# Optimization experiments

Measured on AMD Instinct MI355X. Metric: run time of the kernel, lower is better.

## Reference

```python
import jax, jax.numpy as jnp
import numpy as np


def fwht(x):
    """Normalized fast Walsh-Hadamard transform over the last dim (power of 2).
    Equivalent to x @ H_n / sqrt(n) with H symmetric, so it serves as both
    matmul_hadU and matmul_hadUt in QuIP#."""
    n = x.shape[-1]
    steps = int(np.log2(n))
    assert 1 << steps == n
    shape = x.shape
    x = x.reshape(-1, n)
    h = 1
    for _ in range(steps):
        x = x.reshape(-1, n // (2 * h), 2, h)
        a = x[:, :, 0, :]
        b = x[:, :, 1, :]
        x = jnp.stack([a + b, a - b], axis=2).reshape(-1, n)
        h *= 2
    return (x * np.float32(1.0 / np.sqrt(n))).reshape(shape)


def setup_inputs() -> dict:
    key = jax.random.key(0)
    ks = jax.random.split(key, 9)
    B, S = 4, 2048
    n_in, n_out, codesz, cb_size, rank = 4096, 4096, 4, 256, 64
    inputs = {
        "input": jax.random.normal(ks[0], (B, S, n_in), dtype=jnp.float32),
        "Qidxs": jax.random.randint(ks[1], (n_out, n_in // codesz), 0, cb_size, dtype=jnp.int32),
        "D4_CB": jax.random.normal(ks[2], (cb_size, codesz), dtype=jnp.float32),
        # SU / SV are random sign (+-1) vectors from the randomized Hadamard transform
        "SU": jnp.where(jax.random.bernoulli(ks[3], 0.5, (n_in,)), 1.0, -1.0).astype(jnp.float32),
        "SV": jnp.where(jax.random.bernoulli(ks[4], 0.5, (n_out,)), 1.0, -1.0).astype(jnp.float32),
        "Wscale": jnp.float32(0.9),
        "A": jax.random.normal(ks[5], (n_out, rank), dtype=jnp.float32) * 0.02,
        "B": jax.random.normal(ks[6], (rank, n_in), dtype=jnp.float32) * 0.02,
        # positive per-input-channel rescale
        "scaleWH": jax.random.uniform(ks[7], (n_in,), dtype=jnp.float32, minval=0.5, maxval=1.5),
    }
    return inputs


def reference(input, Qidxs, D4_CB, SU, SV, Wscale, A, B, scaleWH):
    n_out, n_groups = Qidxs.shape
    codesz = D4_CB.shape[1]
    n_in = n_groups * codesz
    lead = input.shape[:-1]

    x = input.reshape(-1, n_in)            # [T, n_in]
    x = x / scaleWH                        # rescale_WH
    x = x * SU                             # input sign flips
    x = fwht(x)                            # matmul_hadUt
    Bx = x @ B.T                           # [T, rank] low-rank path

    # Dequantize: gather codebook vectors and flatten groups -> [n_out, n_in]
    W_hat = D4_CB[Qidxs].reshape(n_out, n_in)
    z = x @ W_hat.T                        # [T, n_out]

    z = z * Wscale
    z = z + Bx @ A.T                       # low-rank correction
    z = fwht(z)                            # matmul_hadU on output dim
    z = z * SV                             # output sign flips
    return z.reshape(*lead, n_out)
```

## Files before the change

kernel.cpp:

```cpp
#include <hip/hip_runtime.h>
#include <hip/hip_bf16.h>
#include <stdint.h>

typedef __attribute__((ext_vector_type(8))) short short8;
typedef __attribute__((ext_vector_type(4))) float floatx4;

#define GLOAD_LDS16(gptr, lptr)                                                     \
  __builtin_amdgcn_global_load_lds(                                                 \
      (const __attribute__((address_space(1))) void*)(gptr),                        \
      (__attribute__((address_space(3))) void*)(lptr), 16, 0, 0)

#define FENCE() asm volatile("" ::: "memory")
#define BARRIER() do { FENCE(); __builtin_amdgcn_s_barrier(); FENCE(); } while (0)
#define PHASE_END() do { __builtin_amdgcn_sched_barrier(0);                        \
                         asm volatile("s_waitcnt lgkmcnt(0)" ::: "memory");        \
                         __builtin_amdgcn_s_barrier();                             \
                         __builtin_amdgcn_sched_barrier(0); } while (0)

__device__ inline void fwht16(float v[16]) {
#pragma unroll
    for (int s = 0; s < 4; ++s) {
        const int h = 1 << s;
#pragma unroll
        for (int k = 0; k < 16; k += 2 * h)
#pragma unroll
            for (int j = 0; j < h; ++j) {
                float a = v[k + j], b = v[k + j + h];
                v[k + j] = a + b;
                v[k + j + h] = a - b;
            }
    }
}

__global__ __launch_bounds__(256) void decode_weff(
    const int* __restrict__ Qidxs, const float* __restrict__ D4_CB,
    const float* __restrict__ Wscale_p, const float* __restrict__ A,
    const float* __restrict__ B, __hip_bfloat16* __restrict__ W_eff)
{
    __shared__ __align__(16) float As[64 * 64];
    __shared__ __align__(16) float CB[256 * 4];
    const int t = threadIdx.x;
    const int oBase = blockIdx.y * 64;
    const int iBase = blockIdx.x * 256;

    const float4* A4 = (const float4*)(A + (long)oBase * 64);
    float4* As4 = (float4*)As;
#pragma unroll
    for (int u = 0; u < 4; ++u) As4[t + u * 256] = A4[t + u * 256];
    ((float4*)CB)[t] = ((const float4*)D4_CB)[t];
    __syncthreads();

    const float wscale = Wscale_p[0];
    const int i = iBase + t;
    float bcol[64];
#pragma unroll
    for (int r = 0; r < 64; ++r) bcol[r] = B[r * 4096 + i];

    const int g = i >> 2;
    const int sub = i & 3;

    for (int oo = 0; oo < 64; ++oo) {
        const int o = oBase + oo;
        const float4* arow = (const float4*)&As[oo * 64];
        float acc = 0.f;
#pragma unroll
        for (int r4 = 0; r4 < 16; ++r4) {
            float4 a4 = arow[r4];
            acc += a4.x * bcol[4 * r4 + 0] + a4.y * bcol[4 * r4 + 1] +
                   a4.z * bcol[4 * r4 + 2] + a4.w * bcol[4 * r4 + 3];
        }
        const int q = Qidxs[(long)o * 1024 + g];
        const float w = wscale * CB[q * 4 + sub] + acc;
        W_eff[(long)o * 4096 + i] = __float2bfloat16(w);
    }
}

__global__ __launch_bounds__(256) void fwht_in_kernel(
    const float* __restrict__ x, const float* __restrict__ SU,
    const float* __restrict__ sWH, __hip_bfloat16* __restrict__ xh)
{
    __shared__ float row[4096 + 256];
    const int t = threadIdx.x;
    const long base = (long)blockIdx.x * 4096;
    float v[16];

#pragma unroll
    for (int u = 0; u < 16; ++u) {
        int e = u * 256 + t;
        v[u] = x[base + e] / sWH[e] * SU[e];
    }
    fwht16(v);
#pragma unroll
    for (int u = 0; u < 16; ++u) {
        int e = u * 256 + t;
        row[e + (e >> 4)] = v[u];
    }
    __syncthreads();

    const int lo = t & 15, hi = t >> 4;
#pragma unroll
    for (int u = 0; u < 16; ++u) v[u] = row[hi * 272 + u * 17 + lo];
    fwht16(v);
#pragma unroll
    for (int u = 0; u < 16; ++u) row[hi * 272 + u * 17 + lo] = v[u];
    __syncthreads();

#pragma unroll
    for (int u = 0; u < 16; ++u) v[u] = row[t * 17 + u];
    fwht16(v);

    short8 o0, o1;
#pragma unroll
    for (int u = 0; u < 8; ++u) {
        __hip_bfloat16 b = __float2bfloat16(v[u] * 0.015625f);
        o0[u] = *(short*)&b;
    }
#pragma unroll
    for (int u = 0; u < 8; ++u) {
        __hip_bfloat16 b = __float2bfloat16(v[8 + u] * 0.015625f);
        o1[u] = *(short*)&b;
    }
    *(short8*)(xh + base + t * 16) = o0;
    *(short8*)(xh + base + t * 16 + 8) = o1;
}

__global__ __launch_bounds__(512, 2) void gemm_bt(
    const __hip_bfloat16* __restrict__ xh,
    const __hip_bfloat16* __restrict__ wf,
    __hip_bfloat16* __restrict__ z)
{
    __shared__ __align__(16) __hip_bfloat16 sA[2][256 * 64];
    __shared__ __align__(16) __hip_bfloat16 sB[2][256 * 64];

    const int t = threadIdx.x;
    const int lane = t & 63;
    const int wv = t >> 6;
    const int wm = wv >> 2;
    const int wn = wv & 3;
    const long mBase = (long)blockIdx.y * 256;
    const long nBase = (long)blockIdx.x * 256;

    const int grow = t >> 3;
    const int gcol = ((t & 7) ^ (grow & 7)) * 8;
    const __hip_bfloat16* gA = xh + (mBase + grow) * 4096 + gcol;
    const __hip_bfloat16* gB = wf + (nBase + grow) * 4096 + gcol;
    const int lrow = wv * 8;

    const int fr = lane & 15;
    const int c2 = lane >> 4;
    const int slot0 = ((c2 ^ (fr & 7)) * 8);

    floatx4 acc[8][4] = {};
    short8 afr[4][2];
    short8 bfr[4][2];

    auto stage = [&](int buf, int isA, int halfRow, int kt) {
        const __hip_bfloat16* g =
            (isA ? gA : gB) + (long)halfRow * 4096 + (long)kt * 64;
        __hip_bfloat16* l =
            (isA ? &sA[buf][0] : &sB[buf][0]) + (halfRow + lrow) * 64;
        GLOAD_LDS16(g, l);
        GLOAD_LDS16(g + 64L * 4096, l + 64 * 64);
    };
    auto ldA = [&](int buf, int mhalf) {
        const __hip_bfloat16* base =
            &sA[buf][0] + (wm * 128 + mhalf * 64 + fr) * 64;
#pragma unroll
        for (int m = 0; m < 4; ++m) {
            afr[m][0] = *(const short8*)(base + m * 16 * 64 + slot0);
            afr[m][1] = *(const short8*)(base + m * 16 * 64 + (slot0 ^ 32));
        }
    };
    auto ldB2 = [&](int buf, int npair) {
        const __hip_bfloat16* base =
            &sB[buf][0] + (wn * 64 + npair * 32 + fr) * 64;
#pragma unroll
        for (int n = 0; n < 2; ++n) {
            bfr[npair * 2 + n][0] = *(const short8*)(base + n * 16 * 64 + slot0);
            bfr[npair * 2 + n][1] = *(const short8*)(base + n * 16 * 64 + (slot0 ^ 32));
        }
    };
    auto mma16 = [&](int mh, int np) {
#pragma unroll
        for (int m = 0; m < 4; ++m)
#pragma unroll
            for (int n = 0; n < 2; ++n)
#pragma unroll
                for (int kh = 0; kh < 2; ++kh)
                    acc[mh * 4 + m][np * 2 + n] =
                        __builtin_amdgcn_mfma_f32_16x16x32_bf16(
                            afr[m][kh], bfr[np * 2 + n][kh],
                            acc[mh * 4 + m][np * 2 + n], 0, 0, 0);
    };

    stage(0, 1, 0,   0);
    stage(0, 1, 128, 0);
    stage(0, 0, 0,   0);
    stage(0, 0, 128, 0);
    stage(1, 0, 0,   1);
    stage(1, 1, 0,   1);
    asm volatile("s_waitcnt vmcnt(4)" ::: "memory");
    BARRIER();

    for (int kt = 0; kt < 64; ++kt) {
        const int cur = kt & 1;

        ldA(cur, 0);
        ldB2(cur, 0);
        if (kt + 1 < 64) stage(cur ^ 1, 1, 128, kt + 1);
        __builtin_amdgcn_s_setprio(1);
        mma16(0, 0);
        __builtin_amdgcn_s_setprio(0);
        PHASE_END();

        ldB2(cur, 1);
        if (kt + 1 < 64) stage(cur ^ 1, 0, 128, kt + 1);
        __builtin_amdgcn_s_setprio(1);
        mma16(0, 1);
        __builtin_amdgcn_s_setprio(0);
        PHASE_END();

        ldA(cur, 1);
        if (kt + 2 < 64) stage(cur, 0, 0, kt + 2);
        __builtin_amdgcn_s_setprio(1);
        mma16(1, 0);
        __builtin_amdgcn_s_setprio(0);
        PHASE_END();

        if (kt + 2 < 64) stage(cur, 1, 0, kt + 2);
        __builtin_amdgcn_s_setprio(1);
        mma16(1, 1);
        __builtin_amdgcn_s_setprio(0);
        __builtin_amdgcn_sched_barrier(0);
        if (kt < 62) asm volatile("s_waitcnt vmcnt(4) lgkmcnt(0)" ::: "memory");
        else         asm volatile("s_waitcnt vmcnt(0) lgkmcnt(0)" ::: "memory");
        __builtin_amdgcn_s_barrier();
        __builtin_amdgcn_sched_barrier(0);
    }

    const int q4 = c2 * 4;
#pragma unroll
    for (int m = 0; m < 8; ++m)
#pragma unroll
        for (int n = 0; n < 4; ++n)
#pragma unroll
            for (int r = 0; r < 4; ++r) {
                const long row = mBase + wm * 128 + m * 16 + q4 + r;
                const long col = nBase + wn * 64 + n * 16 + fr;
                z[row * 4096 + col] = __float2bfloat16(acc[m][n][r]);
            }
}

__global__ __launch_bounds__(256) void fwht_out_kernel(
    const __hip_bfloat16* __restrict__ z, const float* __restrict__ SV,
    float* __restrict__ out)
{
    __shared__ float row[4096 + 256];
    const int t = threadIdx.x;
    const long base = (long)blockIdx.x * 4096;
    float v[16];

#pragma unroll
    for (int u = 0; u < 16; ++u) {
        int e = u * 256 + t;
        v[u] = __bfloat162float(z[base + e]);
    }
    fwht16(v);
#pragma unroll
    for (int u = 0; u < 16; ++u) {
        int e = u * 256 + t;
        row[e + (e >> 4)] = v[u];
    }
    __syncthreads();

    const int lo = t & 15, hi = t >> 4;
#pragma unroll
    for (int u = 0; u < 16; ++u) v[u] = row[hi * 272 + u * 17 + lo];
    fwht16(v);
#pragma unroll
    for (int u = 0; u < 16; ++u) row[hi * 272 + u * 17 + lo] = v[u];
    __syncthreads();

#pragma unroll
    for (int u = 0; u < 16; ++u) v[u] = row[t * 17 + u];
    fwht16(v);

    const float4* svv = (const float4*)(SV + t * 16);
    float4* ov = (float4*)(out + base + t * 16);
#pragma unroll
    for (int c = 0; c < 4; ++c) {
        float4 s = svv[c];
        float4 f;
        f.x = v[4 * c + 0] * s.x * 0.015625f;
        f.y = v[4 * c + 1] * s.y * 0.015625f;
        f.z = v[4 * c + 2] * s.z * 0.015625f;
        f.w = v[4 * c + 3] * s.w * 0.015625f;
        ov[c] = f;
    }
}

extern "C" void kernel_launch(void* const* d_in, const int* in_sizes, int n_in,
                              void* d_out, int out_size, void* d_ws, size_t ws_size,
                              hipStream_t stream)
{
    const float* input  = (const float*)d_in[0];
    const int*   Qidxs  = (const int*)d_in[1];
    const float* D4_CB  = (const float*)d_in[2];
    const float* SU     = (const float*)d_in[3];
    const float* SV     = (const float*)d_in[4];
    const float* Wscale = (const float*)d_in[5];
    const float* A      = (const float*)d_in[6];
    const float* B      = (const float*)d_in[7];
    const float* sWH    = (const float*)d_in[8];
    float* out = (float*)d_out;

    char* ws = (char*)d_ws;
    __hip_bfloat16* weff = (__hip_bfloat16*)ws;
    __hip_bfloat16* xh   = (__hip_bfloat16*)(ws + (32L << 20));
    __hip_bfloat16* zbuf = (__hip_bfloat16*)(ws + (32L << 20) + (64L << 20));

    decode_weff<<<dim3(16, 64), 256, 0, stream>>>(Qidxs, D4_CB, Wscale, A, B, weff);
    fwht_in_kernel<<<8192, 256, 0, stream>>>(input, SU, sWH, xh);
    gemm_bt<<<dim3(16, 32), 512, 0, stream>>>(xh, weff, zbuf);
    fwht_out_kernel<<<8192, 256, 0, stream>>>(zbuf, SV, out);
}
```

Measured before the change: 605.3 us.

## Compute low-rank weight correction with bf16 MFMA in decode kernel

Rewrites the weight-decode kernel so that the rank-64 A@B correction is computed with bf16 MFMA instructions on 256x256 tiles staged in LDS, replacing the per-thread scalar fp32 dot products. The codebook gather and scaling are applied in the epilogue. This cuts the FLOP cost of decode, but A and B are now rounded to bf16 before the product, which changes numerics slightly. The epilogue stores become less coalesced (16 consecutive columns per row).

```diff
diff --git a/kernel.cpp b/kernel.cpp
--- a/kernel.cpp
+++ b/kernel.cpp
@@ -32,47 +32,85 @@
     }
 }
 
-__global__ __launch_bounds__(256) void decode_weff(
+__global__ __launch_bounds__(512) void decode_mfma(
     const int* __restrict__ Qidxs, const float* __restrict__ D4_CB,
     const float* __restrict__ Wscale_p, const float* __restrict__ A,
     const float* __restrict__ B, __hip_bfloat16* __restrict__ W_eff)
 {
-    __shared__ __align__(16) float As[64 * 64];
-    __shared__ __align__(16) float CB[256 * 4];
+    __shared__ __align__(16) __hip_bfloat16 la[256 * 72];
+    __shared__ __align__(16) __hip_bfloat16 lbt[256 * 72];
+    __shared__ __align__(16) float CBs[1024];
+
     const int t = threadIdx.x;
-    const int oBase = blockIdx.y * 64;
-    const int iBase = blockIdx.x * 256;
-
-    const float4* A4 = (const float4*)(A + (long)oBase * 64);
-    float4* As4 = (float4*)As;
-#pragma unroll
-    for (int u = 0; u < 4; ++u) As4[t + u * 256] = A4[t + u * 256];
-    ((float4*)CB)[t] = ((const float4*)D4_CB)[t];
+    const int lane = t & 63;
+    const int wv = t >> 6;
+    const int wm = wv >> 2;
+    const int wn = wv & 3;
+    const long oBase = (long)blockIdx.y * 256;
+    const long iBase = (long)blockIdx.x * 256;
+
+#pragma unroll
+    for (int u = 0; u < 8; ++u) {
+        int el4 = u * 512 + t;
+        int row = el4 >> 4;
+        int r   = (el4 & 15) * 4;
+        float4 v = *(const float4*)(A + (oBase + row) * 64 + r);
+        __hip_bfloat16* d = &la[row * 72 + r];
+        d[0] = __float2bfloat16(v.x); d[1] = __float2bfloat16(v.y);
+        d[2] = __float2bfloat16(v.z); d[3] = __float2bfloat16(v.w);
+    }
+#pragma unroll
+    for (int u = 0; u < 32; ++u) {
+        int el = u * 512 + t;
+        int r = el >> 8;
+        int j = el & 255;
+        lbt[j * 72 + r] = __float2bfloat16(B[(long)r * 4096 + iBase + j]);
+    }
+    if (t < 256) ((float4*)CBs)[t] = ((const float4*)D4_CB)[t];
     __syncthreads();
 
     const float wscale = Wscale_p[0];
-    const int i = iBase + t;
-    float bcol[64];
-#pragma unroll
-    for (int r = 0; r < 64; ++r) bcol[r] = B[r * 4096 + i];
-
-    const int g = i >> 2;
-    const int sub = i & 3;
-
-    for (int oo = 0; oo < 64; ++oo) {
-        const int o = oBase + oo;
-        const float4* arow = (const float4*)&As[oo * 64];
-        float acc = 0.f;
-#pragma unroll
-        for (int r4 = 0; r4 < 16; ++r4) {
-            float4 a4 = arow[r4];
-            acc += a4.x * bcol[4 * r4 + 0] + a4.y * bcol[4 * r4 + 1] +
-                   a4.z * bcol[4 * r4 + 2] + a4.w * bcol[4 * r4 + 3];
-        }
-        const int q = Qidxs[(long)o * 1024 + g];
-        const float w = wscale * CB[q * 4 + sub] + acc;
-        W_eff[(long)o * 4096 + i] = __float2bfloat16(w);
-    }
+    const int fr = lane & 15;
+    const int c2 = lane >> 4;
+    floatx4 acc[8][4] = {};
+    short8 af[4][2], bfx[4][2];
+
+#pragma unroll
+    for (int n = 0; n < 4; ++n)
+#pragma unroll
+        for (int kh = 0; kh < 2; ++kh)
+            bfx[n][kh] = *(const short8*)&lbt[(wn * 64 + n * 16 + fr) * 72 + kh * 32 + c2 * 8];
+
+#pragma unroll
+    for (int mh = 0; mh < 2; ++mh) {
+#pragma unroll
+        for (int m = 0; m < 4; ++m)
+#pragma unroll
+            for (int kh = 0; kh < 2; ++kh)
+                af[m][kh] = *(const short8*)&la[(wm * 128 + mh * 64 + m * 16 + fr) * 72 + kh * 32 + c2 * 8];
+#pragma unroll
+        for (int m = 0; m < 4; ++m)
+#pragma unroll
+            for (int n = 0; n < 4; ++n)
+#pragma unroll
+                for (int kh = 0; kh < 2; ++kh)
+                    acc[mh * 4 + m][n] = __builtin_amdgcn_mfma_f32_16x16x32_bf16(
+                        af[m][kh], bfx[n][kh], acc[mh * 4 + m][n], 0, 0, 0);
+    }
+
+    const int q4 = c2 * 4;
+#pragma unroll
+    for (int m = 0; m < 8; ++m)
+#pragma unroll
+        for (int n = 0; n < 4; ++n)
+#pragma unroll
+            for (int rr = 0; rr < 4; ++rr) {
+                const long o = oBase + wm * 128 + m * 16 + q4 + rr;
+                const long i = iBase + wn * 64 + n * 16 + fr;
+                const int q = Qidxs[o * 1024 + (i >> 2)];
+                const float w = wscale * CBs[q * 4 + (i & 3)] + acc[m][n][rr];
+                W_eff[o * 4096 + i] = __float2bfloat16(w);
+            }
 }
 
 __global__ __launch_bounds__(256) void fwht_in_kernel(
@@ -319,7 +357,7 @@
     __hip_bfloat16* xh   = (__hip_bfloat16*)(ws + (32L << 20));
     __hip_bfloat16* zbuf = (__hip_bfloat16*)(ws + (32L << 20) + (64L << 20));
 
-    decode_weff<<<dim3(16, 64), 256, 0, stream>>>(Qidxs, D4_CB, Wscale, A, B, weff);
+    decode_mfma<<<dim3(16, 16), 512, 0, stream>>>(Qidxs, D4_CB, Wscale, A, B, weff);
     fwht_in_kernel<<<8192, 256, 0, stream>>>(input, SU, sWH, xh);
     gemm_bt<<<dim3(16, 32), 512, 0, stream>>>(xh, weff, zbuf);
     fwht_out_kernel<<<8192, 256, 0, stream>>>(zbuf, SV, out);
```

Result: faster. 552.1 us (-8.8%).
